# Performance work log

Measured on AMD Instinct MI355X. Metric: run time of the kernel, lower is better.

The kernel has to match this reference:

```python
import jax, jax.numpy as jnp
import numpy as np

N = 50000      # nodes
E = 800000     # edges
G = 512        # graphs in the batch
CAT = 32       # node category count
D = 128        # node_emb_dim == gnn_hidden_dim
H = 8          # gat heads
C = 16         # out channels per head (D // H)
EF = 8         # raw edge feature dim
EE = 64        # edge_emb_dim
L = 4          # gnn layers
NCLS = 10
NEG = jnp.float32(-1e9)
BN_EPS = 1e-5


def setup_inputs() -> dict:
    ks = jax.random.split(jax.random.key(0), 24)
    g = lambda k, shape, scale: jax.random.normal(ks[k], shape, jnp.float32) * scale
    return {
        "x_nodes": jax.random.randint(ks[0], (N,), 0, CAT),
        "edge_src": jax.random.randint(ks[1], (E,), 0, N),
        "edge_dst": jax.random.randint(ks[2], (E,), 0, N),
        "edge_attr": g(3, (E, EF), 1.0),
        "batch": jnp.sort(jax.random.randint(ks[4], (N,), 0, G)),
        "node_emb": g(5, (CAT, D), 1.0),
        "edge_W": g(6, (EF, EE), EF ** -0.5),
        "edge_b": jnp.zeros((EE,), jnp.float32),
        "Wl": g(7, (L, D, H * C), D ** -0.5),
        "bl": g(8, (L, H * C), 0.02),
        "Wr": g(9, (L, D, H * C), D ** -0.5),
        "br": g(10, (L, H * C), 0.02),
        "We": g(11, (L, EE, H * C), EE ** -0.5),
        "att": g(12, (L, H, C), C ** -0.5),
        "gbias": g(13, (L, H * C), 0.02),
        "bn_gamma": 1.0 + g(14, (L, H * C), 0.05),
        "bn_beta": g(15, (L, H * C), 0.02),
        "head_W": g(16, (D, NCLS), D ** -0.5),
        "head_b": jnp.zeros((NCLS,), jnp.float32),
    }


def reference(x_nodes, edge_src, edge_dst, edge_attr, batch, node_emb,
              edge_W, edge_b, Wl, bl, Wr, br, We, att, gbias,
              bn_gamma, bn_beta, head_W, head_b):
    x = node_emb[x_nodes]                                    # [N, D] node encoder
    eattr = edge_attr @ edge_W + edge_b                      # [E, EE] edge encoder

    # GATv2Conv add_self_loops: remove existing self loops (masking keeps static
    # shapes), then append one self loop per node with edge_attr = per-node mean
    # of incoming edge attrs (PyG fill_value='mean').
    mask = edge_src != edge_dst                              # [E]
    w = mask.astype(jnp.float32)[:, None]
    cnt = jnp.clip(jax.ops.segment_sum(w, edge_dst, N), 1.0)
    loop_attr = jax.ops.segment_sum(eattr * w, edge_dst, N) / cnt  # [N, EE]
    ea = jnp.concatenate([eattr, loop_attr], axis=0)         # [E+N, EE]
    idx = jnp.arange(N)
    s = jnp.concatenate([edge_src, idx])                     # [E+N]
    d = jnp.concatenate([edge_dst, idx])
    mall = jnp.concatenate([mask, jnp.ones((N,), bool)])

    for i in range(L):
        xl = (x @ Wl[i] + bl[i]).reshape(N, H, C)            # source transform
        xr = (x @ Wr[i] + br[i]).reshape(N, H, C)            # target transform
        ep = (ea @ We[i]).reshape(-1, H, C)                  # edge transform
        z = jax.nn.leaky_relu(xl[s] + xr[d] + ep, 0.2)       # [E+N, H, C]
        logits = jnp.einsum('ehc,hc->eh', z, att[i])         # [E+N, H]
        logits = jnp.where(mall[:, None], logits, NEG)
        # segment softmax over target node d (each node has a self loop -> nonempty)
        m = jax.ops.segment_max(logits, d, num_segments=N)   # [N, H]
        p = jnp.where(mall[:, None], jnp.exp(logits - m[d]), 0.0)
        alpha = p / jax.ops.segment_sum(p, d, N)[d]          # [E+N, H]
        h = jax.ops.segment_sum(alpha[..., None] * xl[s], d, N)  # [N, H, C]
        h = h.reshape(N, H * C) + gbias[i]
        # BatchNorm1d in eval mode with running stats (mean=0, var=1)
        h = bn_gamma[i] * h * (1.0 + BN_EPS) ** -0.5 + bn_beta[i]
        x = jax.nn.elu(h)                                    # dropout inactive (eval)

    # global mean pool over graphs
    gsum = jax.ops.segment_sum(x, batch, G)                  # [G, D]
    gcnt = jnp.clip(jax.ops.segment_sum(jnp.ones((N, 1), jnp.float32), batch, G), 1.0)
    return (gsum / gcnt) @ head_W + head_b                   # [G, NCLS]
```

## Files before the change

kernel.cpp:

```cpp
#include <hip/hip_runtime.h>
#include <hip/hip_fp16.h>
#include <math.h>

static constexpr int N  = 50000;
static constexpr int E  = 800000;
static constexpr int G  = 512;
static constexpr int D  = 128;
static constexpr int EF = 8;
static constexpr int EE = 64;
static constexpr int L  = 4;
static constexpr int NC = 10;

typedef _Float16 half8 __attribute__((ext_vector_type(8)));
typedef _Float16 h2v  __attribute__((ext_vector_type(2)));
typedef float f32x4 __attribute__((ext_vector_type(4)));

union H4 { float4 f4; h2v h[4]; };

#if __has_builtin(__builtin_amdgcn_fdot2)
#define FDOT2(a, b, c) __builtin_amdgcn_fdot2((a), (b), (c), false)
#else
#define FDOT2(a, b, c) ((float)(a)[0]*(float)(b)[0] + (float)(a)[1]*(float)(b)[1] + (c))
#endif

static constexpr size_t pad64(size_t w){ return (w + 63) & ~size_t(63); }
static constexpr size_t O_CNT     = 0;
static constexpr size_t O_CURSOR  = O_CNT + pad64(N);
static constexpr size_t ZERO_END  = O_CURSOR + pad64(N);
static constexpr size_t O_CSROFF  = ZERO_END;
static constexpr size_t O_BSUM    = O_CSROFF + pad64(N+1);
static constexpr size_t O_CSRSRC  = O_BSUM + 64;
static constexpr size_t O_CSREA   = O_CSRSRC + pad64(E);
static constexpr size_t O_MH      = O_CSREA + pad64((size_t)E*4);
static constexpr size_t O_CFOLD   = O_MH + pad64((size_t)L*512);
static constexpr size_t O_LOOPM   = O_CFOLD + pad64(L*D);
static constexpr size_t O_SELFF   = O_LOOPM + pad64((size_t)N*4);
static constexpr size_t O_WFRAG   = O_SELFF + pad64(N);
static constexpr size_t O_XH      = O_WFRAG + pad64((size_t)L*16384);
static constexpr size_t O_XLH     = O_XH  + pad64((size_t)N*64);
static constexpr size_t O_XRH     = O_XLH + pad64((size_t)N*64);

static constexpr int PB_EMB  = (N * D) / 256;
static constexpr int PB_ZERO = ((int)ZERO_END + 255) / 256;
static constexpr int PB_WCVT = (L * 32768) / 256;
static constexpr int PB_FOLD = L;
static constexpr int PB_TOTAL = PB_EMB + PB_ZERO + PB_WCVT + PB_FOLD;

__global__ __launch_bounds__(256) void prep_kernel(
        const int* __restrict__ xn, const float* __restrict__ emb, __half* __restrict__ xh,
        float* __restrict__ zbase,
        const float* __restrict__ Wl, const float* __restrict__ Wr, _Float16* __restrict__ wfrag,
        const float* __restrict__ edge_W, const float* __restrict__ edge_b,
        const float* __restrict__ We, _Float16* __restrict__ Mh, float* __restrict__ cfold) {
    int bid = blockIdx.x, t = threadIdx.x;
    if (bid < PB_EMB) {
        int i = bid * 256 + t;
        int n = i >> 7, c = i & 127;
        xh[i] = __float2half_rn(emb[xn[n] * D + c]);
    } else if (bid < PB_EMB + PB_ZERO) {
        int i = (bid - PB_EMB) * 256 + t;
        if (i < (int)ZERO_END) zbase[i] = 0.0f;
    } else if (bid < PB_EMB + PB_ZERO + PB_WCVT) {
        int i = (bid - PB_EMB - PB_ZERO) * 256 + t;
        int j    = i & 7;
        int lane = (i >> 3) & 63;
        int nt   = (i >> 9) & 15;
        int kt   = (i >> 13) & 3;
        int l    = i >> 15;
        int k = kt * 32 + (lane >> 4) * 8 + j;
        int n = nt * 16 + (lane & 15);
        float v = (n < 128) ? Wl[((size_t)l * D + k) * D + n]
                            : Wr[((size_t)l * D + k) * D + (n - 128)];
        wfrag[i] = (_Float16)v;
    } else {
        int l = bid - PB_EMB - PB_ZERO - PB_WCVT;
        if (t >= 128) return;
        const float* Wel = We + (size_t)l * EE * D;
        for (int j = 0; j < EF; ++j) {
            float s = 0.f;
            for (int k = 0; k < EE; ++k) s += edge_W[j * EE + k] * Wel[k * D + t];
            Mh[((size_t)l * D + t) * 8 + j] = (_Float16)s;
        }
        float s = 0.f;
        for (int k = 0; k < EE; ++k) s += edge_b[k] * Wel[k * D + t];
        cfold[l * D + t] = s;
    }
}

__global__ void edge_cnt_kernel(const int* __restrict__ src, const int* __restrict__ dst,
                                int* __restrict__ cnt) {
    int e = blockIdx.x * blockDim.x + threadIdx.x;
    if (e >= E) return;
    if (src[e] != dst[e]) atomicAdd(&cnt[dst[e]], 1);
}

__global__ void scan1_kernel(const int* __restrict__ cnt, int* __restrict__ out ,
                             int* __restrict__ bsum) {
    __shared__ int lds[256];
    int b = blockIdx.x, t = threadIdx.x;
    int base = b * 1024 + t * 4;
    int v[4]; int s = 0;
    #pragma unroll
    for (int k = 0; k < 4; ++k) { int idx = base + k; v[k] = (idx < N) ? cnt[idx] : 0; s += v[k]; }
    lds[t] = s; __syncthreads();
    for (int off = 1; off < 256; off <<= 1) {
        int add = (t >= off) ? lds[t - off] : 0;
        __syncthreads();
        lds[t] += add;
        __syncthreads();
    }
    int run = (t > 0) ? lds[t - 1] : 0;
    #pragma unroll
    for (int k = 0; k < 4; ++k) { run += v[k]; int idx = base + k; if (idx < N) out[idx] = run; }
    if (t == 255) bsum[b] = lds[255];
}

__global__ void scan3_kernel(int* __restrict__ csr_off, const int* __restrict__ bsum) {
    int i = blockIdx.x * blockDim.x + threadIdx.x;
    if (i == 0) csr_off[0] = 0;
    if (i >= N) return;
    int b = i >> 10;
    int add = 0;
    for (int k = 0; k < b; ++k) add += bsum[k];
    csr_off[1 + i] += add;
}

__global__ void csr_fill_kernel(const int* __restrict__ src, const int* __restrict__ dst,
                                const float* __restrict__ eattr,
                                const int* __restrict__ csr_off, int* __restrict__ cursor,
                                int* __restrict__ csr_src, __half* __restrict__ csr_ea) {
    int e = blockIdx.x * blockDim.x + threadIdx.x;
    if (e >= E) return;
    int s = src[e], d = dst[e];
    if (s == d) return;
    int pos = csr_off[d] + atomicAdd(&cursor[d], 1);
    csr_src[pos] = s << 8;
    const float4* p = reinterpret_cast<const float4*>(eattr + (size_t)e * 8);
    float4 a = p[0], b = p[1];
    __half2 h[4];
    h[0] = __floats2half2_rn(a.x, a.y); h[1] = __floats2half2_rn(a.z, a.w);
    h[2] = __floats2half2_rn(b.x, b.y); h[3] = __floats2half2_rn(b.z, b.w);
    *reinterpret_cast<float4*>(csr_ea + (size_t)pos * 8) = *reinterpret_cast<const float4*>(h);
}

__global__ void loopmean_kernel(const int* __restrict__ csr_off, const __half* __restrict__ csr_ea,
                                __half* __restrict__ loopm, float* __restrict__ selff) {
    int i = blockIdx.x * blockDim.x + threadIdx.x;
    int n = i >> 3, j = i & 7;
    if (n >= N) return;
    int beg = csr_off[n], end = csr_off[n + 1];
    float s = 0.f;
    for (int idx = beg; idx < end; ++idx) s += __half2float(csr_ea[(size_t)idx * 8 + j]);
    int c = end - beg;
    loopm[(size_t)n * 8 + j] = __float2half_rn(s / (float)(c > 1 ? c : 1));
    if (j == 0) selff[n] = (c > 0) ? 1.0f : 0.0f;
}

__global__ __launch_bounds__(256) void transform_kernel(
        const __half* __restrict__ xh, const _Float16* __restrict__ wfrag,
        const float* __restrict__ bl, const float* __restrict__ br,
        __half* __restrict__ xl_h, __half* __restrict__ xr_h) {
    int w = threadIdx.x >> 6, lane = threadIdx.x & 63;
    int quad = lane >> 4, r16 = lane & 15;
    int m0 = blockIdx.x * 16;
    const _Float16* xrow = reinterpret_cast<const _Float16*>(xh) + (size_t)(m0 + r16) * D + quad * 8;
    half8 a[4];
    #pragma unroll
    for (int kt = 0; kt < 4; ++kt) a[kt] = *reinterpret_cast<const half8*>(xrow + kt * 32);
    f32x4 acc[4];
    #pragma unroll
    for (int nt = 0; nt < 4; ++nt) { f32x4 z = {0.f, 0.f, 0.f, 0.f}; acc[nt] = z; }
    #pragma unroll
    for (int nt = 0; nt < 4; ++nt) {
        int ntile = w * 4 + nt;
        #pragma unroll
        for (int kt = 0; kt < 4; ++kt) {
            half8 b = *reinterpret_cast<const half8*>(
                wfrag + ((size_t)(kt * 16 + ntile) * 64 + lane) * 8);
            acc[nt] = __builtin_amdgcn_mfma_f32_16x16x32_f16(a[kt], b, acc[nt], 0, 0, 0);
        }
    }
    #pragma unroll
    for (int nt = 0; nt < 4; ++nt) {
        int n = (w * 4 + nt) * 16 + r16;
        float bias = (n < 128) ? bl[n] : br[n - 128];
        #pragma unroll
        for (int r = 0; r < 4; ++r) {
            int node = m0 + quad * 4 + r;
            float v = acc[nt][r] + bias;
            if (n < 128) xl_h[(size_t)node * D + n] = __float2half_rn(v);
            else         xr_h[(size_t)node * D + (n - 128)] = __float2half_rn(v);
        }
    }
}

__global__ __launch_bounds__(128) void aggregate_kernel(
        const __half* __restrict__ xl_h, const __half* __restrict__ xr_h,
        const __half* __restrict__ loopm, const float* __restrict__ selff,
        const int* __restrict__ csr_off, const int* __restrict__ csr_src,
        const __half* __restrict__ csr_ea,
        const _Float16* __restrict__ Mh, const float* __restrict__ cfold,
        const float* __restrict__ att, const float* __restrict__ gbias,
        const float* __restrict__ bn_gamma, const float* __restrict__ bn_beta,
        __half* __restrict__ xout) {
    int n = blockIdx.x * 2 + (threadIdx.x >> 6);
    int t = threadIdx.x & 63;
    int c0 = t * 2;
    const char* xlb = reinterpret_cast<const char*>(xl_h);
    int lb = t << 2;
    float att0 = att[c0], att1 = att[c0 + 1];
    H4 m0u, m1u;
    m0u.f4 = *reinterpret_cast<const float4*>(Mh + (size_t)c0 * 8);
    m1u.f4 = *reinterpret_cast<const float4*>(Mh + (size_t)(c0 + 1) * 8);
    float cf0 = cfold[c0], cf1 = cfold[c0 + 1];
    float2 xrv = __half22float2(*reinterpret_cast<const __half2*>(xr_h + (size_t)n * D + c0));
    float2 xlv = __half22float2(*reinterpret_cast<const __half2*>(xl_h + (size_t)n * D + c0));

    H4 lau;
    lau.f4 = *reinterpret_cast<const float4*>(loopm + (size_t)n * 8);
    float sf = selff[n];
    float ep0 = cf0 * sf, ep1 = cf1 * sf;
    #pragma unroll
    for (int k = 0; k < 4; ++k) { ep0 = FDOT2(lau.h[k], m0u.h[k], ep0); ep1 = FDOT2(lau.h[k], m1u.h[k], ep1); }
    float z0 = xlv.x + xrv.x + ep0; z0 = fmaxf(z0, 0.2f * z0);
    float z1 = xlv.y + xrv.y + ep1; z1 = fmaxf(z1, 0.2f * z1);
    float lg = z0 * att0 + z1 * att1;
    lg += __shfl_xor(lg, 1); lg += __shfl_xor(lg, 2); lg += __shfl_xor(lg, 4);
    float m = lg, denom = 1.0f, acc0 = xlv.x, acc1 = xlv.y;

    int beg = csr_off[n], end = csr_off[n + 1];
    for (int base = beg; base < end; base += 64) {
        int cnt = end - base; if (cnt > 64) cnt = 64;
        int sreg = (t < cnt) ? csr_src[base + t] : 0;
        int i = 0;
        for (; i + 4 <= cnt; i += 4) {
            int o0 = __shfl(sreg, i),     o1 = __shfl(sreg, i + 1);
            int o2 = __shfl(sreg, i + 2), o3 = __shfl(sreg, i + 3);
            __half2 g0 = *reinterpret_cast<const __half2*>(xlb + o0 + lb);
            __half2 g1 = *reinterpret_cast<const __half2*>(xlb + o1 + lb);
            __half2 g2 = *reinterpret_cast<const __half2*>(xlb + o2 + lb);
            __half2 g3 = *reinterpret_cast<const __half2*>(xlb + o3 + lb);
            H4 e0u, e1u, e2u, e3u;
            e0u.f4 = *reinterpret_cast<const float4*>(csr_ea + (size_t)(base + i) * 8);
            e1u.f4 = *reinterpret_cast<const float4*>(csr_ea + (size_t)(base + i) * 8 + 8);
            e2u.f4 = *reinterpret_cast<const float4*>(csr_ea + (size_t)(base + i) * 8 + 16);
            e3u.f4 = *reinterpret_cast<const float4*>(csr_ea + (size_t)(base + i) * 8 + 24);
            float p00 = cf0, p01 = cf1, p10 = cf0, p11 = cf1;
            float p20 = cf0, p21 = cf1, p30 = cf0, p31 = cf1;
            #pragma unroll
            for (int k = 0; k < 4; ++k) {
                p00 = FDOT2(e0u.h[k], m0u.h[k], p00); p01 = FDOT2(e0u.h[k], m1u.h[k], p01);
                p10 = FDOT2(e1u.h[k], m0u.h[k], p10); p11 = FDOT2(e1u.h[k], m1u.h[k], p11);
                p20 = FDOT2(e2u.h[k], m0u.h[k], p20); p21 = FDOT2(e2u.h[k], m1u.h[k], p21);
                p30 = FDOT2(e3u.h[k], m0u.h[k], p30); p31 = FDOT2(e3u.h[k], m1u.h[k], p31);
            }
            float2 x0 = __half22float2(g0), x1 = __half22float2(g1);
            float2 x2 = __half22float2(g2), x3 = __half22float2(g3);
            float za, zb, l0, l1, l2, l3;
            za = x0.x + xrv.x + p00; za = fmaxf(za, 0.2f * za);
            zb = x0.y + xrv.y + p01; zb = fmaxf(zb, 0.2f * zb);
            l0 = za * att0 + zb * att1;
            za = x1.x + xrv.x + p10; za = fmaxf(za, 0.2f * za);
            zb = x1.y + xrv.y + p11; zb = fmaxf(zb, 0.2f * zb);
            l1 = za * att0 + zb * att1;
            za = x2.x + xrv.x + p20; za = fmaxf(za, 0.2f * za);
            zb = x2.y + xrv.y + p21; zb = fmaxf(zb, 0.2f * zb);
            l2 = za * att0 + zb * att1;
            za = x3.x + xrv.x + p30; za = fmaxf(za, 0.2f * za);
            zb = x3.y + xrv.y + p31; zb = fmaxf(zb, 0.2f * zb);
            l3 = za * att0 + zb * att1;
            l0 += __shfl_xor(l0, 1); l0 += __shfl_xor(l0, 2); l0 += __shfl_xor(l0, 4);
            l1 += __shfl_xor(l1, 1); l1 += __shfl_xor(l1, 2); l1 += __shfl_xor(l1, 4);
            l2 += __shfl_xor(l2, 1); l2 += __shfl_xor(l2, 2); l2 += __shfl_xor(l2, 4);
            l3 += __shfl_xor(l3, 1); l3 += __shfl_xor(l3, 2); l3 += __shfl_xor(l3, 4);
            float nm = fmaxf(fmaxf(m, fmaxf(l0, l1)), fmaxf(l2, l3));
            float wo = __expf(m - nm);
            float w0 = __expf(l0 - nm), w1 = __expf(l1 - nm);
            float w2 = __expf(l2 - nm), w3 = __expf(l3 - nm);
            denom = denom * wo + (w0 + w1) + (w2 + w3);
            acc0 = acc0 * wo + w0 * x0.x + w1 * x1.x + w2 * x2.x + w3 * x3.x;
            acc1 = acc1 * wo + w0 * x0.y + w1 * x1.y + w2 * x2.y + w3 * x3.y;
            m = nm;
        }
        for (; i < cnt; ++i) {
            int o0 = __shfl(sreg, i);
            __half2 g0 = *reinterpret_cast<const __half2*>(xlb + o0 + lb);
            H4 e0u;
            e0u.f4 = *reinterpret_cast<const float4*>(csr_ea + (size_t)(base + i) * 8);
            float p00 = cf0, p01 = cf1;
            #pragma unroll
            for (int k = 0; k < 4; ++k) { p00 = FDOT2(e0u.h[k], m0u.h[k], p00); p01 = FDOT2(e0u.h[k], m1u.h[k], p01); }
            float2 x0 = __half22float2(g0);
            float za = x0.x + xrv.x + p00; za = fmaxf(za, 0.2f * za);
            float zb = x0.y + xrv.y + p01; zb = fmaxf(zb, 0.2f * zb);
            float l0 = za * att0 + zb * att1;
            l0 += __shfl_xor(l0, 1); l0 += __shfl_xor(l0, 2); l0 += __shfl_xor(l0, 4);
            float nm = fmaxf(m, l0);
            float wo = __expf(m - nm), w0 = __expf(l0 - nm);
            denom = denom * wo + w0;
            acc0 = acc0 * wo + w0 * x0.x;
            acc1 = acc1 * wo + w0 * x0.y;
            m = nm;
        }
    }
    float inv = 1.0f / denom;
    float h0 = acc0 * inv + gbias[c0];
    float h1 = acc1 * inv + gbias[c0 + 1];
    h0 = bn_gamma[c0] * h0 * 0.999995000037499813f + bn_beta[c0];
    h1 = bn_gamma[c0 + 1] * h1 * 0.999995000037499813f + bn_beta[c0 + 1];
    h0 = h0 > 0.f ? h0 : (__expf(h0) - 1.0f);
    h1 = h1 > 0.f ? h1 : (__expf(h1) - 1.0f);
    *reinterpret_cast<__half2*>(xout + (size_t)n * D + c0) = __floats2half2_rn(h0, h1);
}

__device__ __forceinline__ int lower_bound_dev(const int* a, int n, int v) {
    int lo = 0, hi = n;
    while (lo < hi) { int mid = (lo + hi) >> 1; if (a[mid] < v) lo = mid + 1; else hi = mid; }
    return lo;
}

__global__ __launch_bounds__(128) void headpool_kernel(
        const __half* __restrict__ xh, const int* __restrict__ batch,
        const float* __restrict__ hW, const float* __restrict__ hb,
        float* __restrict__ out) {
    __shared__ float lds[128];
    int g = blockIdx.x, t = threadIdx.x;
    int lo = lower_bound_dev(batch, N, g);
    int hi = lower_bound_dev(batch, N, g + 1);
    float s = 0.f;
    #pragma unroll 4
    for (int i = lo; i < hi; ++i) s += __half2float(xh[(size_t)i * D + t]);
    int c = hi - lo;
    lds[t] = s / (float)(c > 1 ? c : 1);
    __syncthreads();
    if (t < NC) {
        float p = hb[t];
        #pragma unroll 8
        for (int cc = 0; cc < D; ++cc) p += lds[cc] * hW[cc * NC + t];
        out[g * NC + t] = p;
    }
}

extern "C" void kernel_launch(void* const* d_in, const int* in_sizes, int n_in,
                              void* d_out, int out_size, void* d_ws, size_t ws_size,
                              hipStream_t stream) {
    const int*   x_nodes   = (const int*)  d_in[0];
    const int*   edge_src  = (const int*)  d_in[1];
    const int*   edge_dst  = (const int*)  d_in[2];
    const float* edge_attr = (const float*)d_in[3];
    const int*   batch     = (const int*)  d_in[4];
    const float* node_emb  = (const float*)d_in[5];
    const float* edge_W    = (const float*)d_in[6];
    const float* edge_b    = (const float*)d_in[7];
    const float* Wl        = (const float*)d_in[8];
    const float* bl        = (const float*)d_in[9];
    const float* Wr        = (const float*)d_in[10];
    const float* br        = (const float*)d_in[11];
    const float* We        = (const float*)d_in[12];
    const float* att       = (const float*)d_in[13];
    const float* gbias     = (const float*)d_in[14];
    const float* bn_gamma  = (const float*)d_in[15];
    const float* bn_beta   = (const float*)d_in[16];
    const float* head_W    = (const float*)d_in[17];
    const float* head_b    = (const float*)d_in[18];
    float* out = (float*)d_out;

    float* ws = (float*)d_ws;
    int*    cnt      = (int*)(ws + O_CNT);
    int*    cursor   = (int*)(ws + O_CURSOR);
    int*    csr_off  = (int*)(ws + O_CSROFF);
    int*    bsum     = (int*)(ws + O_BSUM);
    int*    csr_src  = (int*)(ws + O_CSRSRC);
    __half* csr_ea   = (__half*)(ws + O_CSREA);
    _Float16* Mh     = (_Float16*)(ws + O_MH);
    float*  cfold    = ws + O_CFOLD;
    __half* loopm    = (__half*)(ws + O_LOOPM);
    float*  selff    = ws + O_SELFF;
    _Float16* wfrag  = (_Float16*)(ws + O_WFRAG);
    __half* xh   = (__half*)(ws + O_XH);
    __half* xl_h = (__half*)(ws + O_XLH);
    __half* xr_h = (__half*)(ws + O_XRH);

    prep_kernel<<<PB_TOTAL, 256, 0, stream>>>(x_nodes, node_emb, xh, ws,
                                              Wl, Wr, wfrag, edge_W, edge_b, We, Mh, cfold);
    edge_cnt_kernel<<<(E + 255) / 256, 256, 0, stream>>>(edge_src, edge_dst, cnt);
    {
        int nb = (N + 1023) / 1024;
        scan1_kernel<<<nb, 256, 0, stream>>>(cnt, csr_off + 1, bsum);
        scan3_kernel<<<(N + 255) / 256, 256, 0, stream>>>(csr_off, bsum);
    }
    csr_fill_kernel<<<(E + 255) / 256, 256, 0, stream>>>(edge_src, edge_dst, edge_attr,
                                                         csr_off, cursor, csr_src, csr_ea);
    loopmean_kernel<<<(N * 8 + 255) / 256, 256, 0, stream>>>(csr_off, csr_ea, loopm, selff);
    for (int l = 0; l < L; ++l) {
        transform_kernel<<<N / 16, 256, 0, stream>>>(
            xh, wfrag + (size_t)l * 32768, bl + l * D, br + l * D, xl_h, xr_h);
        aggregate_kernel<<<N / 2, 128, 0, stream>>>(
            xl_h, xr_h, loopm, selff, csr_off, csr_src, csr_ea,
            Mh + (size_t)l * D * 8, cfold + l * D, att + l * D, gbias + l * D,
            bn_gamma + l * D, bn_beta + l * D, xh);
    }
    headpool_kernel<<<G, 128, 0, stream>>>(xh, batch, head_W, head_b, out);

    (void)in_sizes; (void)n_in; (void)out_size; (void)ws_size;
}
```

Before: 577.0 us.

## Use packed fp16 math, DPP reductions and exp2 in GAT aggregation

```diff
diff --git a/kernel.cpp b/kernel.cpp
--- a/kernel.cpp
+++ b/kernel.cpp
@@ -13,6 +13,7 @@
 
 typedef _Float16 half8 __attribute__((ext_vector_type(8)));
 typedef _Float16 h2v  __attribute__((ext_vector_type(2)));
+typedef float f2v __attribute__((ext_vector_type(2)));
 typedef float f32x4 __attribute__((ext_vector_type(4)));
 
 union H4 { float4 f4; h2v h[4]; };
@@ -22,6 +23,39 @@
 #else
 #define FDOT2(a, b, c) ((float)(a)[0]*(float)(b)[0] + (float)(a)[1]*(float)(b)[1] + (c))
 #endif
+
+__device__ __forceinline__ h2v pkrtz(float a, float b) {
+    return (h2v)__builtin_amdgcn_cvt_pkrtz(a, b);
+}
+__device__ __forceinline__ h2v hmax2(h2v a, h2v b) {
+#if __has_builtin(__builtin_elementwise_max)
+    return __builtin_elementwise_max(a, b);
+#else
+    h2v r; r[0] = a[0] > b[0] ? a[0] : b[0]; r[1] = a[1] > b[1] ? a[1] : b[1]; return r;
+#endif
+}
+__device__ __forceinline__ h2v hfma2(h2v a, h2v b, h2v c) {
+#if __has_builtin(__builtin_elementwise_fma)
+    return __builtin_elementwise_fma(a, b, c);
+#else
+    return a * b + c;
+#endif
+}
+__device__ __forceinline__ float red8(float v) {
+#if __has_builtin(__builtin_amdgcn_update_dpp)
+    v += __builtin_bit_cast(float, __builtin_amdgcn_update_dpp(
+            0, __builtin_bit_cast(int, v), 0xB1, 0xF, 0xF, true));
+    v += __builtin_bit_cast(float, __builtin_amdgcn_update_dpp(
+            0, __builtin_bit_cast(int, v), 0x4E, 0xF, 0xF, true));
+    v += __builtin_bit_cast(float, __builtin_amdgcn_update_dpp(
+            0, __builtin_bit_cast(int, v), 0x141, 0xF, 0xF, true));
+#else
+    v += __shfl_xor(v, 1); v += __shfl_xor(v, 2); v += __shfl_xor(v, 4);
+#endif
+    return v;
+}
+
+#define LOG2E 1.44269504088896340736f
 
 static constexpr size_t pad64(size_t w){ return (w + 63) & ~size_t(63); }
 static constexpr size_t O_CNT     = 0;
@@ -194,7 +228,7 @@
     }
 }
 
-__global__ __launch_bounds__(128) void aggregate_kernel(
+__global__ __launch_bounds__(64) void aggregate_kernel(
         const __half* __restrict__ xl_h, const __half* __restrict__ xr_h,
         const __half* __restrict__ loopm, const float* __restrict__ selff,
         const int* __restrict__ csr_off, const int* __restrict__ csr_src,
@@ -203,18 +237,19 @@
         const float* __restrict__ att, const float* __restrict__ gbias,
         const float* __restrict__ bn_gamma, const float* __restrict__ bn_beta,
         __half* __restrict__ xout) {
-    int n = blockIdx.x * 2 + (threadIdx.x >> 6);
-    int t = threadIdx.x & 63;
+    int n = blockIdx.x;
+    int t = threadIdx.x;
     int c0 = t * 2;
     const char* xlb = reinterpret_cast<const char*>(xl_h);
     int lb = t << 2;
-    float att0 = att[c0], att1 = att[c0 + 1];
+    h2v attp = pkrtz(att[c0] * LOG2E, att[c0 + 1] * LOG2E);
     H4 m0u, m1u;
     m0u.f4 = *reinterpret_cast<const float4*>(Mh + (size_t)c0 * 8);
     m1u.f4 = *reinterpret_cast<const float4*>(Mh + (size_t)(c0 + 1) * 8);
     float cf0 = cfold[c0], cf1 = cfold[c0 + 1];
-    float2 xrv = __half22float2(*reinterpret_cast<const __half2*>(xr_h + (size_t)n * D + c0));
-    float2 xlv = __half22float2(*reinterpret_cast<const __half2*>(xl_h + (size_t)n * D + c0));
+    h2v xrp = *reinterpret_cast<const h2v*>(xr_h + (size_t)n * D + c0);
+    h2v xlp = *reinterpret_cast<const h2v*>(xl_h + (size_t)n * D + c0);
+    const h2v c02 = {(_Float16)0.2f, (_Float16)0.2f};
 
     H4 lau;
     lau.f4 = *reinterpret_cast<const float4*>(loopm + (size_t)n * 8);
@@ -222,11 +257,16 @@
     float ep0 = cf0 * sf, ep1 = cf1 * sf;
     #pragma unroll
     for (int k = 0; k < 4; ++k) { ep0 = FDOT2(lau.h[k], m0u.h[k], ep0); ep1 = FDOT2(lau.h[k], m1u.h[k], ep1); }
-    float z0 = xlv.x + xrv.x + ep0; z0 = fmaxf(z0, 0.2f * z0);
-    float z1 = xlv.y + xrv.y + ep1; z1 = fmaxf(z1, 0.2f * z1);
-    float lg = z0 * att0 + z1 * att1;
-    lg += __shfl_xor(lg, 1); lg += __shfl_xor(lg, 2); lg += __shfl_xor(lg, 4);
-    float m = lg, denom = 1.0f, acc0 = xlv.x, acc1 = xlv.y;
+    {
+        f2v xlf = __builtin_convertvector(xlp, f2v);
+        f2v xrf = __builtin_convertvector(xrp, f2v);
+        float z0 = xlf[0] + xrf[0] + ep0; z0 = fmaxf(z0, 0.2f * z0);
+        float z1 = xlf[1] + xrf[1] + ep1; z1 = fmaxf(z1, 0.2f * z1);
+        ep0 = FDOT2(pkrtz(z0, z1), attp, 0.0f);
+    }
+    float m = red8(ep0);
+    float denom = 1.0f;
+    h2v acc = xlp;
 
     int beg = csr_off[n], end = csr_off[n + 1];
     for (int base = beg; base < end; base += 64) {
@@ -236,10 +276,10 @@
         for (; i + 4 <= cnt; i += 4) {
             int o0 = __shfl(sreg, i),     o1 = __shfl(sreg, i + 1);
             int o2 = __shfl(sreg, i + 2), o3 = __shfl(sreg, i + 3);
-            __half2 g0 = *reinterpret_cast<const __half2*>(xlb + o0 + lb);
-            __half2 g1 = *reinterpret_cast<const __half2*>(xlb + o1 + lb);
-            __half2 g2 = *reinterpret_cast<const __half2*>(xlb + o2 + lb);
-            __half2 g3 = *reinterpret_cast<const __half2*>(xlb + o3 + lb);
+            h2v g0 = *reinterpret_cast<const h2v*>(xlb + o0 + lb);
+            h2v g1 = *reinterpret_cast<const h2v*>(xlb + o1 + lb);
+            h2v g2 = *reinterpret_cast<const h2v*>(xlb + o2 + lb);
+            h2v g3 = *reinterpret_cast<const h2v*>(xlb + o3 + lb);
             H4 e0u, e1u, e2u, e3u;
             e0u.f4 = *reinterpret_cast<const float4*>(csr_ea + (size_t)(base + i) * 8);
             e1u.f4 = *reinterpret_cast<const float4*>(csr_ea + (size_t)(base + i) * 8 + 8);
@@ -254,58 +294,55 @@
                 p20 = FDOT2(e2u.h[k], m0u.h[k], p20); p21 = FDOT2(e2u.h[k], m1u.h[k], p21);
                 p30 = FDOT2(e3u.h[k], m0u.h[k], p30); p31 = FDOT2(e3u.h[k], m1u.h[k], p31);
             }
-            float2 x0 = __half22float2(g0), x1 = __half22float2(g1);
-            float2 x2 = __half22float2(g2), x3 = __half22float2(g3);
-            float za, zb, l0, l1, l2, l3;
-            za = x0.x + xrv.x + p00; za = fmaxf(za, 0.2f * za);
-            zb = x0.y + xrv.y + p01; zb = fmaxf(zb, 0.2f * zb);
-            l0 = za * att0 + zb * att1;
-            za = x1.x + xrv.x + p10; za = fmaxf(za, 0.2f * za);
-            zb = x1.y + xrv.y + p11; zb = fmaxf(zb, 0.2f * zb);
-            l1 = za * att0 + zb * att1;
-            za = x2.x + xrv.x + p20; za = fmaxf(za, 0.2f * za);
-            zb = x2.y + xrv.y + p21; zb = fmaxf(zb, 0.2f * zb);
-            l2 = za * att0 + zb * att1;
-            za = x3.x + xrv.x + p30; za = fmaxf(za, 0.2f * za);
-            zb = x3.y + xrv.y + p31; zb = fmaxf(zb, 0.2f * zb);
-            l3 = za * att0 + zb * att1;
-            l0 += __shfl_xor(l0, 1); l0 += __shfl_xor(l0, 2); l0 += __shfl_xor(l0, 4);
-            l1 += __shfl_xor(l1, 1); l1 += __shfl_xor(l1, 2); l1 += __shfl_xor(l1, 4);
-            l2 += __shfl_xor(l2, 1); l2 += __shfl_xor(l2, 2); l2 += __shfl_xor(l2, 4);
-            l3 += __shfl_xor(l3, 1); l3 += __shfl_xor(l3, 2); l3 += __shfl_xor(l3, 4);
-            float nm = fmaxf(fmaxf(m, fmaxf(l0, l1)), fmaxf(l2, l3));
-            float wo = __expf(m - nm);
-            float w0 = __expf(l0 - nm), w1 = __expf(l1 - nm);
-            float w2 = __expf(l2 - nm), w3 = __expf(l3 - nm);
+            h2v z0 = g0 + xrp + pkrtz(p00, p01);
+            h2v z1 = g1 + xrp + pkrtz(p10, p11);
+            h2v z2 = g2 + xrp + pkrtz(p20, p21);
+            h2v z3 = g3 + xrp + pkrtz(p30, p31);
+            z0 = hmax2(z0, z0 * c02); z1 = hmax2(z1, z1 * c02);
+            z2 = hmax2(z2, z2 * c02); z3 = hmax2(z3, z3 * c02);
+            float l0 = red8(FDOT2(z0, attp, 0.0f));
+            float l1 = red8(FDOT2(z1, attp, 0.0f));
+            float l2 = red8(FDOT2(z2, attp, 0.0f));
+            float l3 = red8(FDOT2(z3, attp, 0.0f));
+            float gm = fmaxf(fmaxf(l0, l1), fmaxf(l2, l3));
+            float nm = fmaxf(m, gm);
+            float wo = __builtin_amdgcn_exp2f(m - nm);
+            float w0 = __builtin_amdgcn_exp2f(l0 - nm);
+            float w1 = __builtin_amdgcn_exp2f(l1 - nm);
+            float w2 = __builtin_amdgcn_exp2f(l2 - nm);
+            float w3 = __builtin_amdgcn_exp2f(l3 - nm);
             denom = denom * wo + (w0 + w1) + (w2 + w3);
-            acc0 = acc0 * wo + w0 * x0.x + w1 * x1.x + w2 * x2.x + w3 * x3.x;
-            acc1 = acc1 * wo + w0 * x0.y + w1 * x1.y + w2 * x2.y + w3 * x3.y;
+            acc = acc * pkrtz(wo, wo);
+            acc = hfma2(pkrtz(w0, w0), g0, acc);
+            acc = hfma2(pkrtz(w1, w1), g1, acc);
+            acc = hfma2(pkrtz(w2, w2), g2, acc);
+            acc = hfma2(pkrtz(w3, w3), g3, acc);
             m = nm;
         }
         for (; i < cnt; ++i) {
             int o0 = __shfl(sreg, i);
-            __half2 g0 = *reinterpret_cast<const __half2*>(xlb + o0 + lb);
+            h2v g0 = *reinterpret_cast<const h2v*>(xlb + o0 + lb);
             H4 e0u;
             e0u.f4 = *reinterpret_cast<const float4*>(csr_ea + (size_t)(base + i) * 8);
             float p00 = cf0, p01 = cf1;
             #pragma unroll
             for (int k = 0; k < 4; ++k) { p00 = FDOT2(e0u.h[k], m0u.h[k], p00); p01 = FDOT2(e0u.h[k], m1u.h[k], p01); }
-            float2 x0 = __half22float2(g0);
-            float za = x0.x + xrv.x + p00; za = fmaxf(za, 0.2f * za);
-            float zb = x0.y + xrv.y + p01; zb = fmaxf(zb, 0.2f * zb);
-            float l0 = za * att0 + zb * att1;
-            l0 += __shfl_xor(l0, 1); l0 += __shfl_xor(l0, 2); l0 += __shfl_xor(l0, 4);
+            h2v z0 = g0 + xrp + pkrtz(p00, p01);
+            z0 = hmax2(z0, z0 * c02);
+            float l0 = red8(FDOT2(z0, attp, 0.0f));
             float nm = fmaxf(m, l0);
-            float wo = __expf(m - nm), w0 = __expf(l0 - nm);
+            float wo = __builtin_amdgcn_exp2f(m - nm);
+            float w0 = __builtin_amdgcn_exp2f(l0 - nm);
             denom = denom * wo + w0;
-            acc0 = acc0 * wo + w0 * x0.x;
-            acc1 = acc1 * wo + w0 * x0.y;
+            acc = acc * pkrtz(wo, wo);
+            acc = hfma2(pkrtz(w0, w0), g0, acc);
             m = nm;
         }
     }
+    f2v accf = __builtin_convertvector(acc, f2v);
     float inv = 1.0f / denom;
-    float h0 = acc0 * inv + gbias[c0];
-    float h1 = acc1 * inv + gbias[c0 + 1];
+    float h0 = accf[0] * inv + gbias[c0];
+    float h1 = accf[1] * inv + gbias[c0 + 1];
     h0 = bn_gamma[c0] * h0 * 0.999995000037499813f + bn_beta[c0];
     h1 = bn_gamma[c0 + 1] * h1 * 0.999995000037499813f + bn_beta[c0 + 1];
     h0 = h0 > 0.f ? h0 : (__expf(h0) - 1.0f);
@@ -395,7 +432,7 @@
     for (int l = 0; l < L; ++l) {
         transform_kernel<<<N / 16, 256, 0, stream>>>(
             xh, wfrag + (size_t)l * 32768, bl + l * D, br + l * D, xl_h, xr_h);
-        aggregate_kernel<<<N / 2, 128, 0, stream>>>(
+        aggregate_kernel<<<N, 64, 0, stream>>>(
             xl_h, xr_h, loopm, selff, csr_off, csr_src, csr_ea,
             Mh + (size_t)l * D * 8, cfold + l * D, att + l * D, gbias + l * D,
             bn_gamma + l * D, bn_beta + l * D, xh);
```

Measured after the change: 532.9 us. 1.08x faster.
